# Kernel optimization log

Measured on AMD Instinct MI355X. Metric: run time of the kernel, lower is better.

The kernel has to match this reference:

```python
import jax, jax.numpy as jnp
import numpy as np

N_NODES = 100000
N_EDGES = 3200000
D_IN = 128
D_OUT = 128


def setup_inputs() -> dict:
    key = jax.random.key(0)
    k1, k2, k3 = jax.random.split(key, 3)
    x = jax.random.normal(k1, (N_NODES, D_IN), dtype=jnp.float32)
    edge_index = jax.random.randint(k2, (2, N_EDGES), 0, N_NODES, dtype=jnp.int64)
    # Glorot-style init for GCN weight
    W = jax.random.normal(k3, (D_IN, D_OUT), dtype=jnp.float32) * (1.0 / np.sqrt(D_IN))
    b = jnp.zeros((D_OUT,), dtype=jnp.float32)
    return {"x": x, "edge_index": edge_index, "W": W, "b": b}


def reference(x, edge_index, W, b):
    # GCNConv (PyG semantics): add self-loops, symmetric normalization
    # D^-1/2 A D^-1/2, linear transform, aggregate, add bias; then ReLU.
    N = x.shape[0]
    loops = jnp.arange(N, dtype=edge_index.dtype)
    row = jnp.concatenate([edge_index[0], loops])  # source nodes
    col = jnp.concatenate([edge_index[1], loops])  # target nodes
    # degree over targets, with self-loop weight 1
    deg = jax.ops.segment_sum(jnp.ones_like(col, dtype=x.dtype), col,
                              num_segments=N)
    dinv = jnp.where(deg > 0, 1.0 / jnp.sqrt(deg), 0.0)
    norm = dinv[row] * dinv[col]                   # [E+N]
    xl = x @ W                                     # [N, D_OUT] dense GEMM
    msgs = xl[row] * norm[:, None]                 # gather + scale  [E+N, D_OUT]
    agg = jax.ops.segment_sum(msgs, col, num_segments=N)  # scatter-add
    return jax.nn.relu(agg + b)
```

## Files before the change

### kernel.cpp

```cpp
#include <hip/hip_runtime.h>
#include <hip/hip_bf16.h>
#include <math.h>

#define DF 128
#define TILE_EDGES 6144
#define NPB 256
#define NB_MAX 512
#define KP 136

typedef __hip_bfloat16 bf16;
typedef __hip_bfloat162 bf16x2;
typedef __attribute__((ext_vector_type(8))) short short8;
typedef __attribute__((ext_vector_type(4))) float f32x4;

__device__ inline short bf16bits(float f) {
    __hip_bfloat16 h = __float2bfloat16(f);
    return *reinterpret_cast<short*>(&h);
}

__global__ __launch_bounds__(512) void k_binc(const int* __restrict__ col,
                                              int* __restrict__ counts,
                                              int E, int T, int NB) {
    __shared__ int h[NB_MAX];
    int tid = threadIdx.x;
    for (int i = tid; i < NB; i += 512) h[i] = 0;
    __syncthreads();
    int tileBase = blockIdx.x * TILE_EDGES;
    for (int j = 0; j < TILE_EDGES / 512; ++j) {
        int e = tileBase + j * 512 + tid;
        if (e < E) atomicAdd(&h[col[e] >> 8], 1);
    }
    __syncthreads();
    for (int b = tid; b < NB; b += 512)
        counts[b * T + blockIdx.x] = h[b];
}

__global__ __launch_bounds__(256) void k_scanA(int* __restrict__ data,
                                               int* __restrict__ blockSums, int M) {
    __shared__ int tmp[256];
    int tid = threadIdx.x;
    int n = blockIdx.x * 256 + tid;
    int v = (n < M) ? data[n] : 0;
    tmp[tid] = v;
    __syncthreads();
    for (int off = 1; off < 256; off <<= 1) {
        int t = (tid >= off) ? tmp[tid - off] : 0;
        __syncthreads();
        tmp[tid] += t;
        __syncthreads();
    }
    if (tid == 255) blockSums[blockIdx.x] = tmp[255];
    if (n < M) data[n] = tmp[tid] - v;
}

__global__ __launch_bounds__(1024) void k_scanB(int* __restrict__ blockSums, int nb) {
    __shared__ int tmp[1024];
    int tid = threadIdx.x;
    int v = (tid < nb) ? blockSums[tid] : 0;
    tmp[tid] = v;
    __syncthreads();
    for (int off = 1; off < 1024; off <<= 1) {
        int t = (tid >= off) ? tmp[tid - off] : 0;
        __syncthreads();
        tmp[tid] += t;
        __syncthreads();
    }
    if (tid < nb) blockSums[tid] = tmp[tid] - v;
}

__global__ __launch_bounds__(256) void k_scanC(int* __restrict__ data,
                                               const int* __restrict__ blockSums,
                                               int* __restrict__ bucketBase,
                                               int M, int T, int NB, int E) {
    int n = blockIdx.x * 256 + threadIdx.x;
    if (n >= M) return;
    int v = data[n] + blockSums[n >> 8];
    data[n] = v;
    if (n % T == 0) bucketBase[n / T] = v;
    if (n == 0) bucketBase[NB] = E;
}

__global__ __launch_bounds__(512) void k_binscatter(const int* __restrict__ edge,
                                                    const int* __restrict__ tileOff,
                                                    unsigned* __restrict__ binned,
                                                    int E, int T, int NB) {
    __shared__ int cur[NB_MAX];
    int tid = threadIdx.x;
    int t = blockIdx.x;
    for (int b = tid; b < NB; b += 512) cur[b] = tileOff[b * T + t];
    __syncthreads();
    int tileBase = t * TILE_EDGES;
    for (int j = 0; j < TILE_EDGES / 512; ++j) {
        int e = tileBase + j * 512 + tid;
        if (e < E) {
            int r = edge[e];
            int c = edge[E + e];
            int pos = atomicAdd(&cur[c >> 8], 1);
            binned[pos] = ((unsigned)(c & (NPB - 1)) << 24) | (unsigned)r;
        }
    }
}

__global__ __launch_bounds__(512) void k_bucket(const unsigned* __restrict__ binned,
                                                const int* __restrict__ bucketBase,
                                                int* __restrict__ ssrc,
                                                int* __restrict__ offsets,
                                                int* __restrict__ deg,
                                                float* __restrict__ dinv, int N) {
    __shared__ int h[NPB], sc[NPB], cur[NPB];
    int tid = threadIdx.x;
    int b = blockIdx.x;
    int base = bucketBase[b];
    int cnt = bucketBase[b + 1] - base;
    if (tid < NPB) h[tid] = 0;
    __syncthreads();
    for (int i = tid; i < cnt; i += 512)
        atomicAdd(&h[binned[base + i] >> 24], 1);
    __syncthreads();
    if (tid < NPB) sc[tid] = h[tid];
    __syncthreads();
    for (int off = 1; off < NPB; off <<= 1) {
        int tv = (tid >= off && tid < NPB) ? sc[tid - off] : 0;
        __syncthreads();
        if (tid < NPB) sc[tid] += tv;
        __syncthreads();
    }
    if (tid < NPB) {
        int excl = sc[tid] - h[tid];
        cur[tid] = base + excl;
        int node = b * NPB + tid;
        if (node < N) {
            offsets[node] = base + excl;
            deg[node] = h[tid];
            dinv[node] = rsqrtf((float)(h[tid] + 1));
        }
    }
    __syncthreads();
    for (int i = tid; i < cnt; i += 512) {
        unsigned v = binned[base + i];
        int pos = atomicAdd(&cur[v >> 24], 1);
        ssrc[pos] = (int)(v & 0xFFFFFFu);
    }
}

__global__ __launch_bounds__(256) void k_gemm(const float* __restrict__ x,
                                              const float* __restrict__ W,
                                              const float* __restrict__ dinv,
                                              bf16* __restrict__ y, int N) {
    __shared__ bf16 Wt[DF * KP];
    int tid = threadIdx.x;
    for (int i = tid; i < DF * (DF / 4); i += 256) {
        int k = i >> 5;
        int n4 = (i & 31) * 4;
        float4 w = *(const float4*)(W + k * DF + n4);
        Wt[(n4 + 0) * KP + k] = __float2bfloat16(w.x);
        Wt[(n4 + 1) * KP + k] = __float2bfloat16(w.y);
        Wt[(n4 + 2) * KP + k] = __float2bfloat16(w.z);
        Wt[(n4 + 3) * KP + k] = __float2bfloat16(w.w);
    }
    __syncthreads();

    const int wv = tid >> 6;
    const int lane = tid & 63;
    const int m16 = lane & 15;
    const int q = lane >> 4;
    const int rbase = blockIdx.x * 64 + wv * 16;
    const int arow = min(rbase + m16, N - 1);

    f32x4 acc[8];
#pragma unroll
    for (int nt = 0; nt < 8; ++nt) acc[nt] = (f32x4){0.f, 0.f, 0.f, 0.f};

#pragma unroll
    for (int kc = 0; kc < 4; ++kc) {
        int k0 = kc * 32 + q * 8;
        float4 xa = *(const float4*)(x + (size_t)arow * DF + k0);
        float4 xb = *(const float4*)(x + (size_t)arow * DF + k0 + 4);
        short8 a;
        a[0] = bf16bits(xa.x); a[1] = bf16bits(xa.y);
        a[2] = bf16bits(xa.z); a[3] = bf16bits(xa.w);
        a[4] = bf16bits(xb.x); a[5] = bf16bits(xb.y);
        a[6] = bf16bits(xb.z); a[7] = bf16bits(xb.w);
#pragma unroll
        for (int nt = 0; nt < 8; ++nt) {
            short8 b = *(const short8*)(Wt + (nt * 16 + m16) * KP + k0);
            acc[nt] = __builtin_amdgcn_mfma_f32_16x16x32_bf16(a, b, acc[nt], 0, 0, 0);
        }
    }

#pragma unroll
    for (int r = 0; r < 4; ++r) {
        int orow = rbase + q * 4 + r;
        if (orow < N) {
            float dv = dinv[orow];
#pragma unroll
            for (int nt = 0; nt < 8; ++nt) {
                y[(size_t)orow * DF + nt * 16 + m16] = __float2bfloat16(acc[nt][r] * dv);
            }
        }
    }
}

__global__ __launch_bounds__(256) void k_gather(const bf16x2* __restrict__ y,
                                                const int* __restrict__ ssrc,
                                                const int* __restrict__ offsets,
                                                const int* __restrict__ deg,
                                                const float* __restrict__ dinv,
                                                const float* __restrict__ b,
                                                float* __restrict__ out, int N) {
    int wave = (blockIdx.x * 256 + threadIdx.x) >> 6;
    int lane = threadIdx.x & 63;
    if (wave >= N) return;
    int c = wave;
    int start = offsets[c];
    int d = deg[c];

    float2 acc = __bfloat1622float2(y[(size_t)c * 64 + lane]);

    for (int base = 0; base < d; base += 64) {
        int nb = min(64, d - base);
        int idx = ssrc[start + base + min(lane, nb - 1)];
        int j = 0;
        for (; j + 8 <= nb; j += 8) {
            int r0 = __shfl(idx, j + 0);
            int r1 = __shfl(idx, j + 1);
            int r2 = __shfl(idx, j + 2);
            int r3 = __shfl(idx, j + 3);
            int r4 = __shfl(idx, j + 4);
            int r5 = __shfl(idx, j + 5);
            int r6 = __shfl(idx, j + 6);
            int r7 = __shfl(idx, j + 7);
            float2 v0 = __bfloat1622float2(y[(size_t)r0 * 64 + lane]);
            float2 v1 = __bfloat1622float2(y[(size_t)r1 * 64 + lane]);
            float2 v2 = __bfloat1622float2(y[(size_t)r2 * 64 + lane]);
            float2 v3 = __bfloat1622float2(y[(size_t)r3 * 64 + lane]);
            float2 v4 = __bfloat1622float2(y[(size_t)r4 * 64 + lane]);
            float2 v5 = __bfloat1622float2(y[(size_t)r5 * 64 + lane]);
            float2 v6 = __bfloat1622float2(y[(size_t)r6 * 64 + lane]);
            float2 v7 = __bfloat1622float2(y[(size_t)r7 * 64 + lane]);
            acc.x += ((v0.x + v1.x) + (v2.x + v3.x)) + ((v4.x + v5.x) + (v6.x + v7.x));
            acc.y += ((v0.y + v1.y) + (v2.y + v3.y)) + ((v4.y + v5.y) + (v6.y + v7.y));
        }
        for (; j < nb; ++j) {
            int r = __shfl(idx, j);
            float2 v = __bfloat1622float2(y[(size_t)r * 64 + lane]);
            acc.x += v.x;
            acc.y += v.y;
        }
    }

    float dv = dinv[c];
    float2 bb = *(const float2*)(b + lane * 2);
    float2 o;
    o.x = fmaxf(fmaf(dv, acc.x, bb.x), 0.0f);
    o.y = fmaxf(fmaf(dv, acc.y, bb.y), 0.0f);
    *(float2*)(out + (size_t)c * DF + lane * 2) = o;
}

extern "C" void kernel_launch(void* const* d_in, const int* in_sizes, int n_in,
                              void* d_out, int out_size, void* d_ws, size_t ws_size,
                              hipStream_t stream) {
    const float* x    = (const float*)d_in[0];
    const int*   edge = (const int*)d_in[1];
    const float* W    = (const float*)d_in[2];
    const float* b    = (const float*)d_in[3];
    float*       out  = (float*)d_out;

    const int N = in_sizes[0] / DF;
    const int E = in_sizes[1] / 2;

    const int T  = (E + TILE_EDGES - 1) / TILE_EDGES;
    const int NB = (N + NPB - 1) / NPB;
    const int M  = NB * T;

    bf16*     y          = (bf16*)d_ws;
    int*      deg        = (int*)(y + (size_t)N * DF);
    float*    dinv       = (float*)(deg + N);
    int*      offsets    = (int*)(dinv + N);
    int*      bucketBase = offsets + N;
    int*      blockSums  = bucketBase + NB + 8;
    int*      counts     = blockSums + 1024;
    unsigned* binned     = (unsigned*)(counts + M);
    int*      ssrc       = (int*)(binned + E);

    const int nbM = (M + 255) / 256;

    k_binc<<<T, 512, 0, stream>>>(edge + E, counts, E, T, NB);
    k_scanA<<<nbM, 256, 0, stream>>>(counts, blockSums, M);
    k_scanB<<<1, 1024, 0, stream>>>(blockSums, nbM);
    k_scanC<<<nbM, 256, 0, stream>>>(counts, blockSums, bucketBase, M, T, NB, E);
    k_binscatter<<<T, 512, 0, stream>>>(edge, counts, binned, E, T, NB);
    k_bucket<<<NB, 512, 0, stream>>>(binned, bucketBase, ssrc, offsets, deg, dinv, N);
    k_gemm<<<(N + 63) / 64, 256, 0, stream>>>(x, W, dinv, y, N);
    k_gather<<<(N + 3) / 4, 256, 0, stream>>>((const bf16x2*)y, ssrc, offsets, deg, dinv, b, out, N);
}
```

Baseline: 333.0 us.

## Replace per-tile bucket scan with global atomic cursors; split gather wave into half-waves

The binning preprocessing no longer keeps a bucket-by-tile count matrix with a three-kernel scan. It builds a global per-bucket histogram, scans it in a single block, and has each scatter tile reserve its slots through atomics on global cursors after a local histogram. This cuts kernel launches and scan traffic, at the cost of re-reading the column indices and making the bucket order nondeterministic. Separately, the gather kernel now has each half-wave load a whole 256-byte bf16 row with 8-byte loads, so two neighbor rows are fetched per instruction, and the halves are combined by a cross-lane shuffle at the end.

Result: no change. 337.2 us (+1.3%).

```diff
diff --git a/kernel.cpp b/kernel.cpp
--- a/kernel.cpp
+++ b/kernel.cpp
@@ -18,84 +18,77 @@
     return *reinterpret_cast<short*>(&h);
 }
 
-__global__ __launch_bounds__(512) void k_binc(const int* __restrict__ col,
-                                              int* __restrict__ counts,
-                                              int E, int T, int NB) {
+__device__ inline float4 unpack4(float2 p) {
+    unsigned u0 = __float_as_uint(p.x), u1 = __float_as_uint(p.y);
+    float4 r;
+    r.x = __uint_as_float(u0 << 16);
+    r.y = __uint_as_float(u0 & 0xffff0000u);
+    r.z = __uint_as_float(u1 << 16);
+    r.w = __uint_as_float(u1 & 0xffff0000u);
+    return r;
+}
+
+__global__ __launch_bounds__(512) void k_hist(const int* __restrict__ col,
+                                              int* __restrict__ bucketCnt,
+                                              int E, int NB) {
     __shared__ int h[NB_MAX];
     int tid = threadIdx.x;
     for (int i = tid; i < NB; i += 512) h[i] = 0;
     __syncthreads();
-    int tileBase = blockIdx.x * TILE_EDGES;
-    for (int j = 0; j < TILE_EDGES / 512; ++j) {
-        int e = tileBase + j * 512 + tid;
-        if (e < E) atomicAdd(&h[col[e] >> 8], 1);
-    }
-    __syncthreads();
-    for (int b = tid; b < NB; b += 512)
-        counts[b * T + blockIdx.x] = h[b];
-}
-
-__global__ __launch_bounds__(256) void k_scanA(int* __restrict__ data,
-                                               int* __restrict__ blockSums, int M) {
-    __shared__ int tmp[256];
-    int tid = threadIdx.x;
-    int n = blockIdx.x * 256 + tid;
-    int v = (n < M) ? data[n] : 0;
+    for (int e = blockIdx.x * 512 + tid; e < E; e += gridDim.x * 512)
+        atomicAdd(&h[col[e] >> 8], 1);
+    __syncthreads();
+    for (int i = tid; i < NB; i += 512)
+        if (h[i]) atomicAdd(&bucketCnt[i], h[i]);
+}
+
+__global__ __launch_bounds__(512) void k_scanbkt(const int* __restrict__ bucketCnt,
+                                                 int* __restrict__ bucketBase,
+                                                 int* __restrict__ cursor,
+                                                 int NB, int E) {
+    __shared__ int tmp[512];
+    int tid = threadIdx.x;
+    int v = (tid < NB) ? bucketCnt[tid] : 0;
     tmp[tid] = v;
     __syncthreads();
-    for (int off = 1; off < 256; off <<= 1) {
+    for (int off = 1; off < 512; off <<= 1) {
         int t = (tid >= off) ? tmp[tid - off] : 0;
         __syncthreads();
         tmp[tid] += t;
         __syncthreads();
     }
-    if (tid == 255) blockSums[blockIdx.x] = tmp[255];
-    if (n < M) data[n] = tmp[tid] - v;
-}
-
-__global__ __launch_bounds__(1024) void k_scanB(int* __restrict__ blockSums, int nb) {
-    __shared__ int tmp[1024];
-    int tid = threadIdx.x;
-    int v = (tid < nb) ? blockSums[tid] : 0;
-    tmp[tid] = v;
-    __syncthreads();
-    for (int off = 1; off < 1024; off <<= 1) {
-        int t = (tid >= off) ? tmp[tid - off] : 0;
-        __syncthreads();
-        tmp[tid] += t;
-        __syncthreads();
-    }
-    if (tid < nb) blockSums[tid] = tmp[tid] - v;
-}
-
-__global__ __launch_bounds__(256) void k_scanC(int* __restrict__ data,
-                                               const int* __restrict__ blockSums,
-                                               int* __restrict__ bucketBase,
-                                               int M, int T, int NB, int E) {
-    int n = blockIdx.x * 256 + threadIdx.x;
-    if (n >= M) return;
-    int v = data[n] + blockSums[n >> 8];
-    data[n] = v;
-    if (n % T == 0) bucketBase[n / T] = v;
-    if (n == 0) bucketBase[NB] = E;
+    if (tid < NB) {
+        int excl = tmp[tid] - v;
+        bucketBase[tid] = excl;
+        cursor[tid] = excl;
+    }
+    if (tid == 0) bucketBase[NB] = E;
 }
 
 __global__ __launch_bounds__(512) void k_binscatter(const int* __restrict__ edge,
-                                                    const int* __restrict__ tileOff,
+                                                    int* __restrict__ cursor,
                                                     unsigned* __restrict__ binned,
-                                                    int E, int T, int NB) {
-    __shared__ int cur[NB_MAX];
-    int tid = threadIdx.x;
-    int t = blockIdx.x;
-    for (int b = tid; b < NB; b += 512) cur[b] = tileOff[b * T + t];
-    __syncthreads();
-    int tileBase = t * TILE_EDGES;
+                                                    int E, int NB) {
+    __shared__ int h[NB_MAX];
+    __shared__ int curl[NB_MAX];
+    int tid = threadIdx.x;
+    int tileBase = blockIdx.x * TILE_EDGES;
+    for (int i = tid; i < NB; i += 512) h[i] = 0;
+    __syncthreads();
+    for (int j = 0; j < TILE_EDGES / 512; ++j) {
+        int e = tileBase + j * 512 + tid;
+        if (e < E) atomicAdd(&h[edge[E + e] >> 8], 1);
+    }
+    __syncthreads();
+    for (int i = tid; i < NB; i += 512)
+        curl[i] = h[i] ? atomicAdd(&cursor[i], h[i]) : 0;
+    __syncthreads();
     for (int j = 0; j < TILE_EDGES / 512; ++j) {
         int e = tileBase + j * 512 + tid;
         if (e < E) {
             int r = edge[e];
             int c = edge[E + e];
-            int pos = atomicAdd(&cur[c >> 8], 1);
+            int pos = atomicAdd(&curl[c >> 8], 1);
             binned[pos] = ((unsigned)(c & (NPB - 1)) << 24) | (unsigned)r;
         }
     }
@@ -201,12 +194,12 @@
     }
 }
 
-__global__ __launch_bounds__(256) void k_gather(const bf16x2* __restrict__ y,
+__global__ __launch_bounds__(256) void k_gather(const float* __restrict__ yf,
                                                 const int* __restrict__ ssrc,
                                                 const int* __restrict__ offsets,
                                                 const int* __restrict__ deg,
                                                 const float* __restrict__ dinv,
-                                                const float* __restrict__ b,
+                                                const float* __restrict__ bvec,
                                                 float* __restrict__ out, int N) {
     int wave = (blockIdx.x * 256 + threadIdx.x) >> 6;
     int lane = threadIdx.x & 63;
@@ -214,47 +207,83 @@
     int c = wave;
     int start = offsets[c];
     int d = deg[c];
-
-    float2 acc = __bfloat1622float2(y[(size_t)c * 64 + lane]);
+    int half = lane >> 5;
+    int l32 = lane & 31;
+
+    float4 acc = make_float4(0.f, 0.f, 0.f, 0.f);
+    if (half == 0) {
+        float2 sv = *(const float2*)(yf + (size_t)c * 64 + l32 * 2);
+        acc = unpack4(sv);
+    }
 
     for (int base = 0; base < d; base += 64) {
         int nb = min(64, d - base);
         int idx = ssrc[start + base + min(lane, nb - 1)];
         int j = 0;
-        for (; j + 8 <= nb; j += 8) {
-            int r0 = __shfl(idx, j + 0);
-            int r1 = __shfl(idx, j + 1);
-            int r2 = __shfl(idx, j + 2);
-            int r3 = __shfl(idx, j + 3);
-            int r4 = __shfl(idx, j + 4);
-            int r5 = __shfl(idx, j + 5);
-            int r6 = __shfl(idx, j + 6);
-            int r7 = __shfl(idx, j + 7);
-            float2 v0 = __bfloat1622float2(y[(size_t)r0 * 64 + lane]);
-            float2 v1 = __bfloat1622float2(y[(size_t)r1 * 64 + lane]);
-            float2 v2 = __bfloat1622float2(y[(size_t)r2 * 64 + lane]);
-            float2 v3 = __bfloat1622float2(y[(size_t)r3 * 64 + lane]);
-            float2 v4 = __bfloat1622float2(y[(size_t)r4 * 64 + lane]);
-            float2 v5 = __bfloat1622float2(y[(size_t)r5 * 64 + lane]);
-            float2 v6 = __bfloat1622float2(y[(size_t)r6 * 64 + lane]);
-            float2 v7 = __bfloat1622float2(y[(size_t)r7 * 64 + lane]);
-            acc.x += ((v0.x + v1.x) + (v2.x + v3.x)) + ((v4.x + v5.x) + (v6.x + v7.x));
-            acc.y += ((v0.y + v1.y) + (v2.y + v3.y)) + ((v4.y + v5.y) + (v6.y + v7.y));
-        }
-        for (; j < nb; ++j) {
+        for (; j + 16 <= nb; j += 16) {
+            int ra0 = __shfl(idx, j + 0),  rb0 = __shfl(idx, j + 1);
+            int ra1 = __shfl(idx, j + 2),  rb1 = __shfl(idx, j + 3);
+            int ra2 = __shfl(idx, j + 4),  rb2 = __shfl(idx, j + 5);
+            int ra3 = __shfl(idx, j + 6),  rb3 = __shfl(idx, j + 7);
+            int ra4 = __shfl(idx, j + 8),  rb4 = __shfl(idx, j + 9);
+            int ra5 = __shfl(idx, j + 10), rb5 = __shfl(idx, j + 11);
+            int ra6 = __shfl(idx, j + 12), rb6 = __shfl(idx, j + 13);
+            int ra7 = __shfl(idx, j + 14), rb7 = __shfl(idx, j + 15);
+            int r0 = half ? rb0 : ra0;
+            int r1 = half ? rb1 : ra1;
+            int r2 = half ? rb2 : ra2;
+            int r3 = half ? rb3 : ra3;
+            int r4 = half ? rb4 : ra4;
+            int r5 = half ? rb5 : ra5;
+            int r6 = half ? rb6 : ra6;
+            int r7 = half ? rb7 : ra7;
+            float2 v0 = *(const float2*)(yf + (size_t)r0 * 64 + l32 * 2);
+            float2 v1 = *(const float2*)(yf + (size_t)r1 * 64 + l32 * 2);
+            float2 v2 = *(const float2*)(yf + (size_t)r2 * 64 + l32 * 2);
+            float2 v3 = *(const float2*)(yf + (size_t)r3 * 64 + l32 * 2);
+            float2 v4 = *(const float2*)(yf + (size_t)r4 * 64 + l32 * 2);
+            float2 v5 = *(const float2*)(yf + (size_t)r5 * 64 + l32 * 2);
+            float2 v6 = *(const float2*)(yf + (size_t)r6 * 64 + l32 * 2);
+            float2 v7 = *(const float2*)(yf + (size_t)r7 * 64 + l32 * 2);
+            float4 u0 = unpack4(v0), u1 = unpack4(v1), u2 = unpack4(v2), u3 = unpack4(v3);
+            float4 u4 = unpack4(v4), u5 = unpack4(v5), u6 = unpack4(v6), u7 = unpack4(v7);
+            acc.x += ((u0.x + u1.x) + (u2.x + u3.x)) + ((u4.x + u5.x) + (u6.x + u7.x));
+            acc.y += ((u0.y + u1.y) + (u2.y + u3.y)) + ((u4.y + u5.y) + (u6.y + u7.y));
+            acc.z += ((u0.z + u1.z) + (u2.z + u3.z)) + ((u4.z + u5.z) + (u6.z + u7.z));
+            acc.w += ((u0.w + u1.w) + (u2.w + u3.w)) + ((u4.w + u5.w) + (u6.w + u7.w));
+        }
+        for (; j + 2 <= nb; j += 2) {
+            int ra = __shfl(idx, j), rb = __shfl(idx, j + 1);
+            int r = half ? rb : ra;
+            float2 v = *(const float2*)(yf + (size_t)r * 64 + l32 * 2);
+            float4 u = unpack4(v);
+            acc.x += u.x; acc.y += u.y; acc.z += u.z; acc.w += u.w;
+        }
+        if (j < nb) {
             int r = __shfl(idx, j);
-            float2 v = __bfloat1622float2(y[(size_t)r * 64 + lane]);
-            acc.x += v.x;
-            acc.y += v.y;
-        }
-    }
-
-    float dv = dinv[c];
-    float2 bb = *(const float2*)(b + lane * 2);
-    float2 o;
-    o.x = fmaxf(fmaf(dv, acc.x, bb.x), 0.0f);
-    o.y = fmaxf(fmaf(dv, acc.y, bb.y), 0.0f);
-    *(float2*)(out + (size_t)c * DF + lane * 2) = o;
+            if (half == 0) {
+                float2 v = *(const float2*)(yf + (size_t)r * 64 + l32 * 2);
+                float4 u = unpack4(v);
+                acc.x += u.x; acc.y += u.y; acc.z += u.z; acc.w += u.w;
+            }
+        }
+    }
+
+    acc.x += __shfl_xor(acc.x, 32);
+    acc.y += __shfl_xor(acc.y, 32);
+    acc.z += __shfl_xor(acc.z, 32);
+    acc.w += __shfl_xor(acc.w, 32);
+
+    if (half == 0) {
+        float dv = dinv[c];
+        float4 bb = *(const float4*)(bvec + l32 * 4);
+        float4 o;
+        o.x = fmaxf(fmaf(dv, acc.x, bb.x), 0.0f);
+        o.y = fmaxf(fmaf(dv, acc.y, bb.y), 0.0f);
+        o.z = fmaxf(fmaf(dv, acc.z, bb.z), 0.0f);
+        o.w = fmaxf(fmaf(dv, acc.w, bb.w), 0.0f);
+        *(float4*)(out + (size_t)c * DF + l32 * 4) = o;
+    }
 }
 
 extern "C" void kernel_launch(void* const* d_in, const int* in_sizes, int n_in,
@@ -271,26 +300,22 @@
 
     const int T  = (E + TILE_EDGES - 1) / TILE_EDGES;
     const int NB = (N + NPB - 1) / NPB;
-    const int M  = NB * T;
 
     bf16*     y          = (bf16*)d_ws;
     int*      deg        = (int*)(y + (size_t)N * DF);
     float*    dinv       = (float*)(deg + N);
     int*      offsets    = (int*)(dinv + N);
     int*      bucketBase = offsets + N;
-    int*      blockSums  = bucketBase + NB + 8;
-    int*      counts     = blockSums + 1024;
-    unsigned* binned     = (unsigned*)(counts + M);
+    int*      cursor     = bucketBase + NB_MAX + 8;
+    int*      bucketCnt  = cursor + NB_MAX + 8;
+    unsigned* binned     = (unsigned*)(bucketCnt + NB_MAX + 8);
     int*      ssrc       = (int*)(binned + E);
 
-    const int nbM = (M + 255) / 256;
-
-    k_binc<<<T, 512, 0, stream>>>(edge + E, counts, E, T, NB);
-    k_scanA<<<nbM, 256, 0, stream>>>(counts, blockSums, M);
-    k_scanB<<<1, 1024, 0, stream>>>(blockSums, nbM);
-    k_scanC<<<nbM, 256, 0, stream>>>(counts, blockSums, bucketBase, M, T, NB, E);
-    k_binscatter<<<T, 512, 0, stream>>>(edge, counts, binned, E, T, NB);
+    (void)hipMemsetAsync(bucketCnt, 0, (NB + 1) * sizeof(int), stream);
+    k_hist<<<512, 512, 0, stream>>>(edge + E, bucketCnt, E, NB);
+    k_scanbkt<<<1, 512, 0, stream>>>(bucketCnt, bucketBase, cursor, NB, E);
+    k_binscatter<<<T, 512, 0, stream>>>(edge, cursor, binned, E, NB);
     k_bucket<<<NB, 512, 0, stream>>>(binned, bucketBase, ssrc, offsets, deg, dinv, N);
     k_gemm<<<(N + 63) / 64, 256, 0, stream>>>(x, W, dinv, y, N);
-    k_gather<<<(N + 3) / 4, 256, 0, stream>>>((const bf16x2*)y, ssrc, offsets, deg, dinv, b, out, N);
-}
+    k_gather<<<(N + 3) / 4, 256, 0, stream>>>((const float*)y, ssrc, offsets, deg, dinv, b, out, N);
+}
```

## Fuse bucket sort into gather kernel with LDS neighbor lists and half-wave edges

Applied to the files above, without the earlier changes.

Splits the old bucket kernel into a degree-only pass and moves the per-node counting sort into the gather kernel. Each block sorts its bucket's sources into an LDS list (global fallback when the count exceeds CAP), then gathers with each half-wave handling alternate edges and reading 8 bytes per lane, combined by a cross-half shuffle. This removes the global ssrc write and re-read and the offsets array. The cost is lower occupancy from the large LDS allocation and gather parallelism limited to 8 waves per 256 nodes. It also makes the block-sum scan handle more than 1024 entries.

Measured after the change: 337.6 us. Within noise of the previous version (+1.4%).

```diff
diff --git a/kernel.cpp b/kernel.cpp
--- a/kernel.cpp
+++ b/kernel.cpp
@@ -7,15 +7,25 @@
 #define NPB 256
 #define NB_MAX 512
 #define KP 136
+#define CAP 9216
 
 typedef __hip_bfloat16 bf16;
-typedef __hip_bfloat162 bf16x2;
 typedef __attribute__((ext_vector_type(8))) short short8;
 typedef __attribute__((ext_vector_type(4))) float f32x4;
 
 __device__ inline short bf16bits(float f) {
     __hip_bfloat16 h = __float2bfloat16(f);
     return *reinterpret_cast<short*>(&h);
+}
+
+__device__ inline float4 unpack4(float2 p) {
+    unsigned u0 = __float_as_uint(p.x), u1 = __float_as_uint(p.y);
+    float4 r;
+    r.x = __uint_as_float(u0 << 16);
+    r.y = __uint_as_float(u0 & 0xffff0000u);
+    r.z = __uint_as_float(u1 << 16);
+    r.w = __uint_as_float(u1 & 0xffff0000u);
+    return r;
 }
 
 __global__ __launch_bounds__(512) void k_binc(const int* __restrict__ col,
@@ -56,16 +66,22 @@
 __global__ __launch_bounds__(1024) void k_scanB(int* __restrict__ blockSums, int nb) {
     __shared__ int tmp[1024];
     int tid = threadIdx.x;
-    int v = (tid < nb) ? blockSums[tid] : 0;
-    tmp[tid] = v;
-    __syncthreads();
-    for (int off = 1; off < 1024; off <<= 1) {
-        int t = (tid >= off) ? tmp[tid - off] : 0;
-        __syncthreads();
-        tmp[tid] += t;
-        __syncthreads();
-    }
-    if (tid < nb) blockSums[tid] = tmp[tid] - v;
+    int carry = 0;
+    for (int c0 = 0; c0 < nb; c0 += 1024) {
+        int n = c0 + tid;
+        int v = (n < nb) ? blockSums[n] : 0;
+        tmp[tid] = v;
+        __syncthreads();
+        for (int off = 1; off < 1024; off <<= 1) {
+            int t = (tid >= off) ? tmp[tid - off] : 0;
+            __syncthreads();
+            tmp[tid] += t;
+            __syncthreads();
+        }
+        if (n < nb) blockSums[n] = carry + tmp[tid] - v;
+        carry += tmp[1023];
+        __syncthreads();
+    }
 }
 
 __global__ __launch_bounds__(256) void k_scanC(int* __restrict__ data,
@@ -101,45 +117,24 @@
     }
 }
 
-__global__ __launch_bounds__(512) void k_bucket(const unsigned* __restrict__ binned,
-                                                const int* __restrict__ bucketBase,
-                                                int* __restrict__ ssrc,
-                                                int* __restrict__ offsets,
-                                                int* __restrict__ deg,
-                                                float* __restrict__ dinv, int N) {
-    __shared__ int h[NPB], sc[NPB], cur[NPB];
+__global__ __launch_bounds__(512) void k_deg(const unsigned* __restrict__ binned,
+                                             const int* __restrict__ bucketBase,
+                                             int* __restrict__ deg,
+                                             float* __restrict__ dinv, int N) {
+    __shared__ int h[NPB];
     int tid = threadIdx.x;
     int b = blockIdx.x;
+    if (tid < NPB) h[tid] = 0;
+    __syncthreads();
     int base = bucketBase[b];
     int cnt = bucketBase[b + 1] - base;
-    if (tid < NPB) h[tid] = 0;
-    __syncthreads();
     for (int i = tid; i < cnt; i += 512)
         atomicAdd(&h[binned[base + i] >> 24], 1);
     __syncthreads();
-    if (tid < NPB) sc[tid] = h[tid];
-    __syncthreads();
-    for (int off = 1; off < NPB; off <<= 1) {
-        int tv = (tid >= off && tid < NPB) ? sc[tid - off] : 0;
-        __syncthreads();
-        if (tid < NPB) sc[tid] += tv;
-        __syncthreads();
-    }
-    if (tid < NPB) {
-        int excl = sc[tid] - h[tid];
-        cur[tid] = base + excl;
-        int node = b * NPB + tid;
-        if (node < N) {
-            offsets[node] = base + excl;
-            deg[node] = h[tid];
-            dinv[node] = rsqrtf((float)(h[tid] + 1));
-        }
-    }
-    __syncthreads();
-    for (int i = tid; i < cnt; i += 512) {
-        unsigned v = binned[base + i];
-        int pos = atomicAdd(&cur[v >> 24], 1);
-        ssrc[pos] = (int)(v & 0xFFFFFFu);
+    int node = b * NPB + tid;
+    if (tid < NPB && node < N) {
+        deg[node] = h[tid];
+        dinv[node] = rsqrtf((float)(h[tid] + 1));
     }
 }
 
@@ -201,60 +196,121 @@
     }
 }
 
-__global__ __launch_bounds__(256) void k_gather(const bf16x2* __restrict__ y,
-                                                const int* __restrict__ ssrc,
-                                                const int* __restrict__ offsets,
-                                                const int* __restrict__ deg,
-                                                const float* __restrict__ dinv,
-                                                const float* __restrict__ b,
-                                                float* __restrict__ out, int N) {
-    int wave = (blockIdx.x * 256 + threadIdx.x) >> 6;
-    int lane = threadIdx.x & 63;
-    if (wave >= N) return;
-    int c = wave;
-    int start = offsets[c];
-    int d = deg[c];
-
-    float2 acc = __bfloat1622float2(y[(size_t)c * 64 + lane]);
-
-    for (int base = 0; base < d; base += 64) {
-        int nb = min(64, d - base);
-        int idx = ssrc[start + base + min(lane, nb - 1)];
+__global__ __launch_bounds__(512) void k_gatherfused(
+        const float* __restrict__ yf,
+        const unsigned* __restrict__ binned,
+        const int* __restrict__ bucketBase,
+        const int* __restrict__ deg,
+        const float* __restrict__ bvec,
+        int* __restrict__ ssrcG,
+        float* __restrict__ out, int N) {
+    __shared__ int h[NPB], sc[NPB], cur[NPB];
+    __shared__ int lst[CAP];
+    int tid = threadIdx.x;
+    int b = blockIdx.x;
+    int base = bucketBase[b];
+    int cnt = bucketBase[b + 1] - base;
+    int nodeBase = b * NPB;
+
+    if (tid < NPB) {
+        int node = nodeBase + tid;
+        int d = (node < N) ? deg[node] : 0;
+        h[tid] = d;
+        sc[tid] = d;
+    }
+    __syncthreads();
+    for (int off = 1; off < NPB; off <<= 1) {
+        int tv = (tid >= off && tid < NPB) ? sc[tid - off] : 0;
+        __syncthreads();
+        if (tid < NPB) sc[tid] += tv;
+        __syncthreads();
+    }
+    if (tid < NPB) cur[tid] = sc[tid] - h[tid];
+    __syncthreads();
+
+    const bool inLds = (cnt <= CAP);
+    const int* idxp = inLds ? (const int*)lst : (ssrcG + base);
+    for (int i = tid; i < cnt; i += 512) {
+        unsigned v = binned[base + i];
+        int pos = atomicAdd(&cur[v >> 24], 1);
+        int r = (int)(v & 0xFFFFFFu);
+        if (inLds) lst[pos] = r; else ssrcG[base + pos] = r;
+    }
+    __syncthreads();
+
+    int lane = tid & 63;
+    int wv = tid >> 6;
+    int half = lane >> 5;
+    int l32 = lane & 31;
+
+    for (int t = wv; t < NPB; t += 8) {
+        int c = nodeBase + t;
+        if (c >= N) break;
+        int d = h[t];
+        int ls = sc[t] - d;
+
+        float4 acc = make_float4(0.f, 0.f, 0.f, 0.f);
+        if (half == 0) {
+            float2 sv = *(const float2*)(yf + (size_t)c * 64 + l32 * 2);
+            acc = unpack4(sv);
+        }
+
         int j = 0;
-        for (; j + 8 <= nb; j += 8) {
-            int r0 = __shfl(idx, j + 0);
-            int r1 = __shfl(idx, j + 1);
-            int r2 = __shfl(idx, j + 2);
-            int r3 = __shfl(idx, j + 3);
-            int r4 = __shfl(idx, j + 4);
-            int r5 = __shfl(idx, j + 5);
-            int r6 = __shfl(idx, j + 6);
-            int r7 = __shfl(idx, j + 7);
-            float2 v0 = __bfloat1622float2(y[(size_t)r0 * 64 + lane]);
-            float2 v1 = __bfloat1622float2(y[(size_t)r1 * 64 + lane]);
-            float2 v2 = __bfloat1622float2(y[(size_t)r2 * 64 + lane]);
-            float2 v3 = __bfloat1622float2(y[(size_t)r3 * 64 + lane]);
-            float2 v4 = __bfloat1622float2(y[(size_t)r4 * 64 + lane]);
-            float2 v5 = __bfloat1622float2(y[(size_t)r5 * 64 + lane]);
-            float2 v6 = __bfloat1622float2(y[(size_t)r6 * 64 + lane]);
-            float2 v7 = __bfloat1622float2(y[(size_t)r7 * 64 + lane]);
-            acc.x += ((v0.x + v1.x) + (v2.x + v3.x)) + ((v4.x + v5.x) + (v6.x + v7.x));
-            acc.y += ((v0.y + v1.y) + (v2.y + v3.y)) + ((v4.y + v5.y) + (v6.y + v7.y));
-        }
-        for (; j < nb; ++j) {
-            int r = __shfl(idx, j);
-            float2 v = __bfloat1622float2(y[(size_t)r * 64 + lane]);
-            acc.x += v.x;
-            acc.y += v.y;
-        }
-    }
-
-    float dv = dinv[c];
-    float2 bb = *(const float2*)(b + lane * 2);
-    float2 o;
-    o.x = fmaxf(fmaf(dv, acc.x, bb.x), 0.0f);
-    o.y = fmaxf(fmaf(dv, acc.y, bb.y), 0.0f);
-    *(float2*)(out + (size_t)c * DF + lane * 2) = o;
+        for (; j + 16 <= d; j += 16) {
+            int r0 = idxp[ls + j + 0 + half];
+            int r1 = idxp[ls + j + 2 + half];
+            int r2 = idxp[ls + j + 4 + half];
+            int r3 = idxp[ls + j + 6 + half];
+            int r4 = idxp[ls + j + 8 + half];
+            int r5 = idxp[ls + j + 10 + half];
+            int r6 = idxp[ls + j + 12 + half];
+            int r7 = idxp[ls + j + 14 + half];
+            float2 v0 = *(const float2*)(yf + (size_t)r0 * 64 + l32 * 2);
+            float2 v1 = *(const float2*)(yf + (size_t)r1 * 64 + l32 * 2);
+            float2 v2 = *(const float2*)(yf + (size_t)r2 * 64 + l32 * 2);
+            float2 v3 = *(const float2*)(yf + (size_t)r3 * 64 + l32 * 2);
+            float2 v4 = *(const float2*)(yf + (size_t)r4 * 64 + l32 * 2);
+            float2 v5 = *(const float2*)(yf + (size_t)r5 * 64 + l32 * 2);
+            float2 v6 = *(const float2*)(yf + (size_t)r6 * 64 + l32 * 2);
+            float2 v7 = *(const float2*)(yf + (size_t)r7 * 64 + l32 * 2);
+            float4 u0 = unpack4(v0), u1 = unpack4(v1), u2 = unpack4(v2), u3 = unpack4(v3);
+            float4 u4 = unpack4(v4), u5 = unpack4(v5), u6 = unpack4(v6), u7 = unpack4(v7);
+            acc.x += ((u0.x + u1.x) + (u2.x + u3.x)) + ((u4.x + u5.x) + (u6.x + u7.x));
+            acc.y += ((u0.y + u1.y) + (u2.y + u3.y)) + ((u4.y + u5.y) + (u6.y + u7.y));
+            acc.z += ((u0.z + u1.z) + (u2.z + u3.z)) + ((u4.z + u5.z) + (u6.z + u7.z));
+            acc.w += ((u0.w + u1.w) + (u2.w + u3.w)) + ((u4.w + u5.w) + (u6.w + u7.w));
+        }
+        for (; j + 2 <= d; j += 2) {
+            int r = idxp[ls + j + half];
+            float2 v = *(const float2*)(yf + (size_t)r * 64 + l32 * 2);
+            float4 u = unpack4(v);
+            acc.x += u.x; acc.y += u.y; acc.z += u.z; acc.w += u.w;
+        }
+        if (j < d) {
+            if (half == 0) {
+                int r = idxp[ls + j];
+                float2 v = *(const float2*)(yf + (size_t)r * 64 + l32 * 2);
+                float4 u = unpack4(v);
+                acc.x += u.x; acc.y += u.y; acc.z += u.z; acc.w += u.w;
+            }
+        }
+
+        acc.x += __shfl_xor(acc.x, 32);
+        acc.y += __shfl_xor(acc.y, 32);
+        acc.z += __shfl_xor(acc.z, 32);
+        acc.w += __shfl_xor(acc.w, 32);
+
+        if (half == 0) {
+            float dv = rsqrtf((float)(d + 1));
+            float4 bb = *(const float4*)(bvec + l32 * 4);
+            float4 o;
+            o.x = fmaxf(fmaf(dv, acc.x, bb.x), 0.0f);
+            o.y = fmaxf(fmaf(dv, acc.y, bb.y), 0.0f);
+            o.z = fmaxf(fmaf(dv, acc.z, bb.z), 0.0f);
+            o.w = fmaxf(fmaf(dv, acc.w, bb.w), 0.0f);
+            *(float4*)(out + (size_t)c * DF + l32 * 4) = o;
+        }
+    }
 }
 
 extern "C" void kernel_launch(void* const* d_in, const int* in_sizes, int n_in,
@@ -276,10 +332,9 @@
     bf16*     y          = (bf16*)d_ws;
     int*      deg        = (int*)(y + (size_t)N * DF);
     float*    dinv       = (float*)(deg + N);
-    int*      offsets    = (int*)(dinv + N);
-    int*      bucketBase = offsets + N;
-    int*      blockSums  = bucketBase + NB + 8;
-    int*      counts     = blockSums + 1024;
+    int*      bucketBase = (int*)(dinv + N);
+    int*      blockSums  = bucketBase + NB_MAX + 8;
+    int*      counts     = blockSums + 2048;
     unsigned* binned     = (unsigned*)(counts + M);
     int*      ssrc       = (int*)(binned + E);
 
@@ -290,7 +345,8 @@
     k_scanB<<<1, 1024, 0, stream>>>(blockSums, nbM);
     k_scanC<<<nbM, 256, 0, stream>>>(counts, blockSums, bucketBase, M, T, NB, E);
     k_binscatter<<<T, 512, 0, stream>>>(edge, counts, binned, E, T, NB);
-    k_bucket<<<NB, 512, 0, stream>>>(binned, bucketBase, ssrc, offsets, deg, dinv, N);
+    k_deg<<<NB, 512, 0, stream>>>(binned, bucketBase, deg, dinv, N);
     k_gemm<<<(N + 63) / 64, 256, 0, stream>>>(x, W, dinv, y, N);
-    k_gather<<<(N + 3) / 4, 256, 0, stream>>>((const bf16x2*)y, ssrc, offsets, deg, dinv, b, out, N);
-}
+    k_gatherfused<<<NB, 512, 0, stream>>>((const float*)y, binned, bucketBase, deg,
+                                          b, ssrc, out, N);
+}
```
